# Kernel optimization log

Hardware: AMD Instinct MI355X
Metric: run time of the kernel (lower is better)

## Reference

```python
import jax, jax.numpy as jnp
import numpy as np

N_MODELS = 16
IN_F = 1024
OUT_F = 1024
N_TOK = 8192


def setup_inputs() -> dict:
    key = jax.random.key(0)
    k1, k2, k3, k4 = jax.random.split(key, 4)
    x = jax.random.normal(k1, (N_TOK, IN_F), dtype=jnp.float32)
    idxs = jax.random.randint(k2, (N_TOK,), 0, N_MODELS, dtype=jnp.int64)
    w = jax.random.normal(k3, (N_MODELS, IN_F, OUT_F), dtype=jnp.float32) * 0.02
    b = jax.random.normal(k4, (N_MODELS, OUT_F), dtype=jnp.float32) * 0.02
    return {"x": x, "idxs": idxs, "w": w, "b": b}


def reference(x, idxs, w, b):
    # Equivalent math to the torch loop: for each expert i, tokens with
    # idxs==i get x @ w[i] + b[i]; finally ReLU over all outputs.
    # Loop over the small fixed expert count; selection by mask avoids
    # materializing the [N, E, out] tensor or gathering per-token weights.
    y = jnp.zeros((x.shape[0], w.shape[2]), dtype=x.dtype)
    for i in range(w.shape[0]):
        yi = x @ w[i] + b[i]  # [N, out]
        y = jnp.where((idxs == i)[:, None], yi, y)
    return jax.nn.relu(y)
```

## Files before the change

### kernel.cpp

```cpp
#include <hip/hip_runtime.h>
#include <hip/hip_bf16.h>
#include <stdint.h>

#define N_MODELS 16
#define IN_F 1024
#define OUT_F 1024
#define N_TOK 8192
#define MAX_MT 80

typedef unsigned short u16;
using us4   = __attribute__((ext_vector_type(4))) unsigned short;
using s16x8 = __attribute__((ext_vector_type(8))) short;
using f32x4 = __attribute__((ext_vector_type(4))) float;

__device__ __forceinline__ u16 f2bf(float f) {
    union { float f; uint32_t u; } v;
    v.f = f;
    uint32_t u = v.u;
    u += 0x7fffu + ((u >> 16) & 1u);
    return (u16)(u >> 16);
}

__device__ __forceinline__ void gload16(const u16* g, u16* l) {
    __builtin_amdgcn_global_load_lds(
        (const __attribute__((address_space(1))) void*)g,
        (__attribute__((address_space(3))) void*)l, 16, 0, 0);
}

#define ROW 17
#define WBLOCKS 2048
#define XBLOCKS2 512

__global__ __launch_bounds__(256)
void prep_kernel(const float* __restrict__ w, const float* __restrict__ x,
                 const int* __restrict__ idxs,
                 int* __restrict__ perm,
                 int* __restrict__ offs,
                 int* __restrict__ tile_off,
                 u16* __restrict__ wT, u16* __restrict__ xg)
{
    __shared__ int cnt[256 * ROW];
    __shared__ int offsS[N_MODELS + 1];
    __shared__ int tileS[N_MODELS + 1];
    __shared__ int destS[128];
    int t  = threadIdx.x;
    int bx = blockIdx.x;

    if (bx == 0) {
#pragma unroll
        for (int e = 0; e < N_MODELS; ++e) cnt[t * ROW + e] = 0;
        __syncthreads();

        int base = t * 32;
#pragma unroll
        for (int i = 0; i < 32; ++i) cnt[t * ROW + idxs[base + i]] += 1;
        __syncthreads();

#pragma unroll
        for (int s = 1; s < 256; s <<= 1) {
            int v[N_MODELS];
#pragma unroll
            for (int e = 0; e < N_MODELS; ++e)
                v[e] = (t >= s) ? cnt[(t - s) * ROW + e] : 0;
            __syncthreads();
#pragma unroll
            for (int e = 0; e < N_MODELS; ++e)
                cnt[t * ROW + e] += v[e];
            __syncthreads();
        }

        if (t == 0) {
            int o = 0, to = 0;
            for (int e = 0; e < N_MODELS; ++e) {
                int c = cnt[255 * ROW + e];
                offsS[e] = o;
                offs[e] = o; tile_off[e] = to;
                to += (c + 127) >> 7;
                o  += c;
            }
            offsS[N_MODELS] = o;
            offs[N_MODELS] = o; tile_off[N_MODELS] = to;
        }
        __syncthreads();

        int cur[N_MODELS];
#pragma unroll
        for (int e = 0; e < N_MODELS; ++e)
            cur[e] = offsS[e] + ((t > 0) ? cnt[(t - 1) * ROW + e] : 0);
        __syncthreads();
#pragma unroll
        for (int e = 0; e < N_MODELS; ++e) cnt[t * ROW + e] = cur[e];

#pragma unroll
        for (int i = 0; i < 32; ++i) {
            int tok = base + i;
            int e = idxs[tok];
            perm[cnt[t * ROW + e]++] = tok;
        }
        return;
    }

    if (bx <= WBLOCKS) {
        int wb = bx - 1;
        int e  = wb >> 7;
        int nt = (wb >> 4) & 7;
        int kg = wb & 15;
        int n    = t & 127;
        int half = t >> 7;

        const float* wp = w  + (size_t)e * (IN_F * OUT_F) + (size_t)nt * 128 + n;
        u16*         ob = wT + ((size_t)(e * 8 + nt)) * 131072 + (size_t)n * 8;

#pragma unroll
        for (int i = 0; i < 4; ++i) {
            int kog = kg * 8 + half + i * 2;
            float r[8];
#pragma unroll
            for (int j = 0; j < 8; ++j)
                r[j] = wp[(size_t)(kog * 8 + j) * OUT_F];
            union { __hip_bfloat162 h; uint32_t u; } c0, c1, c2, c3;
            c0.h = __float22bfloat162_rn(make_float2(r[0], r[1]));
            c1.h = __float22bfloat162_rn(make_float2(r[2], r[3]));
            c2.h = __float22bfloat162_rn(make_float2(r[4], r[5]));
            c3.h = __float22bfloat162_rn(make_float2(r[6], r[7]));
            union { s16x8 v; uint32_t u[4]; } outv;
            outv.u[0] = c0.u; outv.u[1] = c1.u; outv.u[2] = c2.u; outv.u[3] = c3.u;
            *(s16x8*)(ob + (size_t)kog * 1024) = outv.v;
        }
        return;
    }

    int bx2 = bx - (WBLOCKS + 1);
    int g   = bx2 >> 3;
    int kg  = bx2 & 7;

#pragma unroll
    for (int e = 0; e < N_MODELS; ++e) cnt[t * ROW + e] = 0;
    __syncthreads();

    int base = t * 32;
#pragma unroll
    for (int i = 0; i < 32; ++i) cnt[t * ROW + idxs[base + i]] += 1;
    __syncthreads();

#pragma unroll
    for (int s = 1; s < 256; s <<= 1) {
        int v[N_MODELS];
#pragma unroll
        for (int e = 0; e < N_MODELS; ++e)
            v[e] = (t >= s) ? cnt[(t - s) * ROW + e] : 0;
        __syncthreads();
#pragma unroll
        for (int e = 0; e < N_MODELS; ++e)
            cnt[t * ROW + e] += v[e];
        __syncthreads();
    }

    if (t == 0) {
        int to = 0;
        for (int e = 0; e < N_MODELS; ++e) {
            tileS[e] = to;
            to += (cnt[255 * ROW + e] + 127) >> 7;
        }
    }
    __syncthreads();

    if (t < 4) {
        int tr = g * 4 + t;
        int curL[N_MODELS];
#pragma unroll
        for (int e = 0; e < N_MODELS; ++e)
            curL[e] = (tr > 0) ? cnt[(tr - 1) * ROW + e] : 0;
        for (int i = 0; i < 32; ++i) {
            int tok = tr * 32 + i;
            int e = idxs[tok];
            destS[t * 32 + i] = (tileS[e] << 7) + curL[e]++;
        }
    }
    __syncthreads();

    int r0   = t >> 3;
    int apos = t & 7;
    int q    = apos >> 1;
    int j0   = (apos & 1) * 4;

#pragma unroll
    for (int kb4 = 0; kb4 < 4; ++kb4) {
        int kb = kg * 4 + kb4;
        int k  = kb * 32 + apos * 4;
#pragma unroll
        for (int i = 0; i < 4; ++i) {
            int lt  = r0 + i * 32;
            int tok = g * 128 + lt;
            int d   = destS[lt];
            const float4 v = *(const float4*)(x + (size_t)tok * IN_F + k);
            us4 pk; pk.x = f2bf(v.x); pk.y = f2bf(v.y); pk.z = f2bf(v.z); pk.w = f2bf(v.w);
            *(us4*)(xg + (size_t)(d >> 7) * 131072 + (size_t)kb * 4096
                       + (size_t)q * 1024 + (d & 127) * 8 + j0) = pk;
        }
    }
}

__global__ __launch_bounds__(256, 3)
void gemm_kernel(const u16* __restrict__ xg, const u16* __restrict__ wT,
                 const float* __restrict__ bias,
                 const int* __restrict__ perm, const int* __restrict__ offs,
                 const int* __restrict__ tile_off,
                 float* __restrict__ out)
{
    __shared__ u16 Bs[2][8192];
    __shared__ int   permS[128];
    __shared__ float biasS[128];
    __shared__ int   toS[N_MODELS + 1];

    int t = threadIdx.x;
    int o    = blockIdx.x;
    int wgid = (o & 7) * MAX_MT + (o >> 3);
    int bt   = wgid >> 3;
    int nt   = wgid & 7;

    if (t <= N_MODELS) toS[t] = tile_off[t];
    __syncthreads();
    if (bt >= toS[N_MODELS]) return;

    int e = 0;
    while (toS[e + 1] <= bt) ++e;
    int s0   = offs[e] + (bt - toS[e]) * 128;
    int sEnd = offs[e + 1];
    int mValid = sEnd - s0; if (mValid > 128) mValid = 128;

    if (t < 128) {
        permS[t] = (s0 + t < sEnd) ? perm[s0 + t] : 0;
        biasS[t] = bias[(size_t)e * OUT_F + nt * 128 + t];
    }

    const u16* atile = xg + (size_t)bt * 131072;
    const u16* btile = wT + ((size_t)(e * 8 + nt)) * 131072;

    int lane = t & 63;
    int wv   = t >> 6;
    int wm   = (wv >> 1) * 64;
    int wn   = (wv & 1) * 64;
    int m    = lane & 15;
    int q    = lane >> 4;

    int aoff = q * 1024 + (wm + m) * 8;
    int boff = q * 1024 + (wn + m) * 8;

    f32x4 acc[4][4];
#pragma unroll
    for (int i = 0; i < 4; ++i)
#pragma unroll
        for (int j = 0; j < 4; ++j)
            acc[i][j] = (f32x4){0.f, 0.f, 0.f, 0.f};

#pragma unroll
    for (int i = 0; i < 4; ++i)
        gload16(btile + wv * 2048 + i * 512 + lane * 8, &Bs[0][wv * 2048 + i * 512]);

    s16x8 a0[4], a1[4];
#pragma unroll
    for (int mt2 = 0; mt2 < 4; ++mt2)
        a0[mt2] = *(const s16x8*)(atile + aoff + mt2 * 128);
#pragma unroll
    for (int mt2 = 0; mt2 < 4; ++mt2)
        a1[mt2] = *(const s16x8*)(atile + 4096 + aoff + mt2 * 128);

    for (int kb2 = 0; kb2 < 16; ++kb2) {
        int cur = kb2 & 1;
        __syncthreads();
        if (kb2 < 15) {
            const u16* gb = btile + (size_t)(kb2 + 1) * 8192;
#pragma unroll
            for (int i = 0; i < 4; ++i)
                gload16(gb + wv * 2048 + i * 512 + lane * 8,
                        &Bs[cur ^ 1][wv * 2048 + i * 512]);
        }
        if (kb2 > 0) {
#pragma unroll
            for (int mt2 = 0; mt2 < 4; ++mt2)
                a1[mt2] = *(const s16x8*)(atile + (size_t)kb2 * 8192 + 4096 + aoff + mt2 * 128);
        }

        s16x8 bf[4];
#pragma unroll
        for (int nt2 = 0; nt2 < 4; ++nt2)
            bf[nt2] = *(const s16x8*)(&Bs[cur][boff + nt2 * 128]);
#pragma unroll
        for (int mt2 = 0; mt2 < 4; ++mt2)
#pragma unroll
            for (int nt2 = 0; nt2 < 4; ++nt2)
                acc[mt2][nt2] = __builtin_amdgcn_mfma_f32_16x16x32_bf16(
                    a0[mt2], bf[nt2], acc[mt2][nt2], 0, 0, 0);

        if (kb2 < 15) {
#pragma unroll
            for (int mt2 = 0; mt2 < 4; ++mt2)
                a0[mt2] = *(const s16x8*)(atile + (size_t)(kb2 + 1) * 8192 + aoff + mt2 * 128);
        }

#pragma unroll
        for (int nt2 = 0; nt2 < 4; ++nt2)
            bf[nt2] = *(const s16x8*)(&Bs[cur][4096 + boff + nt2 * 128]);
#pragma unroll
        for (int mt2 = 0; mt2 < 4; ++mt2)
#pragma unroll
            for (int nt2 = 0; nt2 < 4; ++nt2)
                acc[mt2][nt2] = __builtin_amdgcn_mfma_f32_16x16x32_bf16(
                    a1[mt2], bf[nt2], acc[mt2][nt2], 0, 0, 0);
    }

#pragma unroll
    for (int mt2 = 0; mt2 < 4; ++mt2) {
        int rbase = wm + mt2 * 16 + q * 4;
#pragma unroll
        for (int i = 0; i < 4; ++i) {
            int r = rbase + i;
            if (r < mValid) {
                int tok = permS[r];
                float* orow = out + (size_t)tok * OUT_F + nt * 128;
#pragma unroll
                for (int nt2 = 0; nt2 < 4; ++nt2) {
                    int col = wn + nt2 * 16 + m;
                    float v = acc[mt2][nt2][i] + biasS[col];
                    orow[col] = v > 0.f ? v : 0.f;
                }
            }
        }
    }
}

extern "C" void kernel_launch(void* const* d_in, const int* in_sizes, int n_in,
                              void* d_out, int out_size, void* d_ws, size_t ws_size,
                              hipStream_t stream) {
    const float* x    = (const float*)d_in[0];
    const int*   idxs = (const int*)d_in[1];
    const float* w    = (const float*)d_in[2];
    const float* b    = (const float*)d_in[3];
    float* out = (float*)d_out;

    u16* wT = (u16*)d_ws;
    u16* xg = wT + (size_t)N_MODELS * IN_F * OUT_F;
    int* perm     = (int*)(xg + (size_t)MAX_MT * 32 * 4096);
    int* offs     = perm + N_TOK;
    int* tile_off = offs + (N_MODELS + 1);

    prep_kernel<<<1 + WBLOCKS + XBLOCKS2, 256, 0, stream>>>(
        w, x, idxs, perm, offs, tile_off, wT, xg);
    gemm_kernel<<<8 * MAX_MT, 256, 0, stream>>>(xg, wT, b, perm, offs, tile_off, out);
}
```

Before: 199.2 us.

## Fuse fp32-to-bf16 weight conversion into GEMM B-tile loading

Removes the separate weight transpose/convert pass from the prep kernel. The GEMM now reads fp32 weights directly into registers, packs them to bf16 and stores them into the double-buffered LDS tile, prefetching two k-blocks ahead. This avoids writing and re-reading a 32MB bf16 weight copy. In exchange, every M-tile re-reads fp32 weights, doubling the bytes per tile read. It also adds 32 prefetch registers per thread under a 3-waves occupancy bound, and gives up the async global-to-LDS loads.

```diff
diff --git a/kernel.cpp b/kernel.cpp
--- a/kernel.cpp
+++ b/kernel.cpp
@@ -21,23 +21,27 @@
     return (u16)(u >> 16);
 }
 
-__device__ __forceinline__ void gload16(const u16* g, u16* l) {
-    __builtin_amdgcn_global_load_lds(
-        (const __attribute__((address_space(1))) void*)g,
-        (__attribute__((address_space(3))) void*)l, 16, 0, 0);
+__device__ __forceinline__ s16x8 pack8(const float* r) {
+    union { __hip_bfloat162 h; uint32_t u; } c0, c1, c2, c3;
+    c0.h = __float22bfloat162_rn(make_float2(r[0], r[1]));
+    c1.h = __float22bfloat162_rn(make_float2(r[2], r[3]));
+    c2.h = __float22bfloat162_rn(make_float2(r[4], r[5]));
+    c3.h = __float22bfloat162_rn(make_float2(r[6], r[7]));
+    union { s16x8 v; uint32_t u[4]; } outv;
+    outv.u[0] = c0.u; outv.u[1] = c1.u; outv.u[2] = c2.u; outv.u[3] = c3.u;
+    return outv.v;
 }
 
 #define ROW 17
-#define WBLOCKS 2048
 #define XBLOCKS2 512
 
 __global__ __launch_bounds__(256)
-void prep_kernel(const float* __restrict__ w, const float* __restrict__ x,
-                 const int* __restrict__ idxs,
-                 int* __restrict__ perm,
-                 int* __restrict__ offs,
-                 int* __restrict__ tile_off,
-                 u16* __restrict__ wT, u16* __restrict__ xg)
+void xsetup_kernel(const float* __restrict__ x,
+                   const int* __restrict__ idxs,
+                   int* __restrict__ perm,
+                   int* __restrict__ offs,
+                   int* __restrict__ tile_off,
+                   u16* __restrict__ xg)
 {
     __shared__ int cnt[256 * ROW];
     __shared__ int offsS[N_MODELS + 1];
@@ -100,37 +104,7 @@
         return;
     }
 
-    if (bx <= WBLOCKS) {
-        int wb = bx - 1;
-        int e  = wb >> 7;
-        int nt = (wb >> 4) & 7;
-        int kg = wb & 15;
-        int n    = t & 127;
-        int half = t >> 7;
-
-        const float* wp = w  + (size_t)e * (IN_F * OUT_F) + (size_t)nt * 128 + n;
-        u16*         ob = wT + ((size_t)(e * 8 + nt)) * 131072 + (size_t)n * 8;
-
-#pragma unroll
-        for (int i = 0; i < 4; ++i) {
-            int kog = kg * 8 + half + i * 2;
-            float r[8];
-#pragma unroll
-            for (int j = 0; j < 8; ++j)
-                r[j] = wp[(size_t)(kog * 8 + j) * OUT_F];
-            union { __hip_bfloat162 h; uint32_t u; } c0, c1, c2, c3;
-            c0.h = __float22bfloat162_rn(make_float2(r[0], r[1]));
-            c1.h = __float22bfloat162_rn(make_float2(r[2], r[3]));
-            c2.h = __float22bfloat162_rn(make_float2(r[4], r[5]));
-            c3.h = __float22bfloat162_rn(make_float2(r[6], r[7]));
-            union { s16x8 v; uint32_t u[4]; } outv;
-            outv.u[0] = c0.u; outv.u[1] = c1.u; outv.u[2] = c2.u; outv.u[3] = c3.u;
-            *(s16x8*)(ob + (size_t)kog * 1024) = outv.v;
-        }
-        return;
-    }
-
-    int bx2 = bx - (WBLOCKS + 1);
+    int bx2 = bx - 1;
     int g   = bx2 >> 3;
     int kg  = bx2 & 7;
 
@@ -202,7 +176,7 @@
 }
 
 __global__ __launch_bounds__(256, 3)
-void gemm_kernel(const u16* __restrict__ xg, const u16* __restrict__ wT,
+void gemm_kernel(const u16* __restrict__ xg, const float* __restrict__ w,
                  const float* __restrict__ bias,
                  const int* __restrict__ perm, const int* __restrict__ offs,
                  const int* __restrict__ tile_off,
@@ -235,7 +209,12 @@
     }
 
     const u16* atile = xg + (size_t)bt * 131072;
-    const u16* btile = wT + ((size_t)(e * 8 + nt)) * 131072;
+
+    int n  = t & 127;
+    int kh = t >> 7;
+    const float* wbase = w + (size_t)e * (IN_F * OUT_F) + (size_t)kh * 8 * OUT_F
+                           + (size_t)nt * 128 + n;
+    int n8 = n * 8;
 
     int lane = t & 63;
     int wv   = t >> 6;
@@ -254,9 +233,23 @@
         for (int j = 0; j < 4; ++j)
             acc[i][j] = (f32x4){0.f, 0.f, 0.f, 0.f};
 
+    float fr[4][8];
+
 #pragma unroll
     for (int i = 0; i < 4; ++i)
-        gload16(btile + wv * 2048 + i * 512 + lane * 8, &Bs[0][wv * 2048 + i * 512]);
+#pragma unroll
+        for (int j = 0; j < 8; ++j)
+            fr[i][j] = wbase[(size_t)(i * 16 + j) * OUT_F];
+#pragma unroll
+    for (int i = 0; i < 4; ++i) {
+        int ko = kh + 2 * i;
+        *(s16x8*)(&Bs[0][(ko >> 2) * 4096 + (ko & 3) * 1024 + n8]) = pack8(fr[i]);
+    }
+#pragma unroll
+    for (int i = 0; i < 4; ++i)
+#pragma unroll
+        for (int j = 0; j < 8; ++j)
+            fr[i][j] = wbase[(size_t)(64 + i * 16 + j) * OUT_F];
 
     s16x8 a0[4], a1[4];
 #pragma unroll
@@ -269,12 +262,20 @@
     for (int kb2 = 0; kb2 < 16; ++kb2) {
         int cur = kb2 & 1;
         __syncthreads();
+
         if (kb2 < 15) {
-            const u16* gb = btile + (size_t)(kb2 + 1) * 8192;
+#pragma unroll
+            for (int i = 0; i < 4; ++i) {
+                int ko = kh + 2 * i;
+                *(s16x8*)(&Bs[cur ^ 1][(ko >> 2) * 4096 + (ko & 3) * 1024 + n8]) = pack8(fr[i]);
+            }
+        }
+        if (kb2 < 14) {
 #pragma unroll
             for (int i = 0; i < 4; ++i)
-                gload16(gb + wv * 2048 + i * 512 + lane * 8,
-                        &Bs[cur ^ 1][wv * 2048 + i * 512]);
+#pragma unroll
+                for (int j = 0; j < 8; ++j)
+                    fr[i][j] = wbase[(size_t)((kb2 + 2) * 64 + i * 16 + j) * OUT_F];
         }
         if (kb2 > 0) {
 #pragma unroll
@@ -339,13 +340,11 @@
     const float* b    = (const float*)d_in[3];
     float* out = (float*)d_out;
 
-    u16* wT = (u16*)d_ws;
-    u16* xg = wT + (size_t)N_MODELS * IN_F * OUT_F;
+    u16* xg = (u16*)d_ws;
     int* perm     = (int*)(xg + (size_t)MAX_MT * 32 * 4096);
     int* offs     = perm + N_TOK;
     int* tile_off = offs + (N_MODELS + 1);
 
-    prep_kernel<<<1 + WBLOCKS + XBLOCKS2, 256, 0, stream>>>(
-        w, x, idxs, perm, offs, tile_off, wT, xg);
-    gemm_kernel<<<8 * MAX_MT, 256, 0, stream>>>(xg, wT, b, perm, offs, tile_off, out);
-}
+    xsetup_kernel<<<1 + XBLOCKS2, 256, 0, stream>>>(x, idxs, perm, offs, tile_off, xg);
+    gemm_kernel<<<8 * MAX_MT, 256, 0, stream>>>(xg, w, b, perm, offs, tile_off, out);
+}
```

New measurement: 183.1 us. 1.09x faster.
